# Performance work log

Hardware: AMD Instinct MI355X
Metric: run time of the kernel (lower is better)

## Reference

```python
import jax, jax.numpy as jnp
import numpy as np

D, HID, C = 300, 64, 21          # Dict_size, hidden_size, cell_size
B, H, W = 4, 144, 144

def gelu(x):
    return jax.nn.gelu(x, approximate=False)  # torch nn.GELU default (erf)

def c1x1(x, w, b):
    # 1x1 conv == pointwise matmul over channels: x [b,c,h,w], w [o,c], b [o]
    return jnp.einsum('bchw,oc->bohw', x, w) + b[None, :, None, None]

def gconv(x, w, b):
    return gelu(c1x1(x, w, b))


def setup_inputs() -> dict:
    key = jax.random.key(0)
    ks = iter(jax.random.split(key, 40))
    def Wm(o, i):
        return jax.random.normal(next(ks), (o, i), jnp.float32) * 0.05
    def bv(o):
        return jax.random.normal(next(ks), (o,), jnp.float32) * 0.01
    inp = {'y': jax.random.normal(next(ks), (B, C, H, W), jnp.float32)}
    # cell_size -> Dict_size encoders
    for nm in ['we1', 'we2', 'wfy1', 'wiy1', 'wfy2', 'wiy2']:
        inp[nm + '_w'] = Wm(D, C); inp[nm + '_b'] = bv(D)
    # Dict_size -> Dict_size recurrent convs
    for nm in ['wd1', 'wd2', 'wfx1', 'wix1', 'wfx2', 'wix2']:
        inp[nm + '_w'] = Wm(D, D); inp[nm + '_b'] = bv(D)
    # Line1 head: 3x3 valid conv D->2*HID, then 1x1 2*HID->2*HID, 1x1 2*HID->1
    inp['line_w1'] = jax.random.normal(next(ks), (2 * HID, D, 3, 3), jnp.float32) * 0.05
    inp['line_b1'] = bv(2 * HID)
    inp['line_w2'] = Wm(2 * HID, 2 * HID); inp['line_b2'] = bv(2 * HID)
    inp['line_w3'] = Wm(1, 2 * HID);       inp['line_b3'] = bv(1)
    return inp


def reference(y, we1_w, we1_b, we2_w, we2_b, wfy1_w, wfy1_b, wiy1_w, wiy1_b,
              wfy2_w, wfy2_b, wiy2_w, wiy2_b, wd1_w, wd1_b, wd2_w, wd2_b,
              wfx1_w, wfx1_b, wix1_w, wix1_b, wfx2_w, wfx2_b, wix2_w, wix2_b,
              line_w1, line_b1, line_w2, line_b2, line_w3, line_b3):
    ywe1 = gconv(y, we1_w, we1_b)
    ywe2 = gconv(y, we2_w, we2_b)
    ywfy1 = gconv(y, wfy1_w, wfy1_b)
    ywiy1 = gconv(y, wiy1_w, wiy1_b)
    ywfy2 = gconv(y, wfy2_w, wfy2_b)
    ywiy2 = gconv(y, wiy2_w, wiy2_b)

    def step2(x12, c12, xt1):  # first half-cell (the '2' gates)
        ctlide1 = ywe2 + xt1 - gconv(x12, wd2_w, wd2_b)
        ft1 = jax.nn.sigmoid(gconv(x12, wfx2_w, wfx2_b) + ywfy2)
        it1 = jax.nn.sigmoid(gconv(x12, wix2_w, wix2_b) + ywiy2)
        ct1 = c12 * ft1 + ctlide1 * it1
        return ct1, jax.nn.relu(ct1)

    xt1 = jnp.float32(0.0)
    c12 = jax.nn.sigmoid(ywiy1) * (-ywe1)
    x12 = jax.nn.relu(c12)

    for _ in range(3):
        ct1, xt1 = step2(x12, c12, xt1)
        c1tlide = ywe1 + xt1 - gconv(xt1, wd1_w, wd1_b)
        ft21 = jax.nn.sigmoid(gconv(xt1, wfx1_w, wfx1_b) + ywfy1)
        it21 = jax.nn.sigmoid(gconv(xt1, wix1_w, wix1_b) + ywiy1)
        ct2 = ct1 * ft21 + c1tlide * it21
        x12 = jax.nn.relu(ct2)
        c12 = ct2

    ct1, xt1 = step2(x12, c12, xt1)

    # Line1: 3x3 valid conv + GELU, 1x1 + GELU, 1x1
    h = jax.lax.conv_general_dilated(
        xt1, line_w1, window_strides=(1, 1), padding='VALID',
        dimension_numbers=('NCHW', 'OIHW', 'NCHW')) + line_b1[None, :, None, None]
    h = gelu(h)
    h = gelu(c1x1(h, line_w2, line_b2))
    return c1x1(h, line_w3, line_b3)
```

## Files before the change

kernel.cpp:

```cpp
#include <hip/hip_runtime.h>

typedef _Float16 f16;
typedef _Float16 f16x8 __attribute__((ext_vector_type(8)));
typedef _Float16 f16x4 __attribute__((ext_vector_type(4)));
typedef float    f32x4 __attribute__((ext_vector_type(4)));

#define NP      82944
#define NPIX_B  20736
#define KP      320
#define OC      128
#define NP2     80656
#define NOC     15
#define OCH     20

__device__ __forceinline__ float geluf(float x) {
    return 0.5f * x * (1.0f + erff(x * 0.70710678118654752f));
}
__device__ __forceinline__ float sigm(float x) {
    return 1.0f / (1.0f + __expf(-x));
}
__device__ __forceinline__ f32x4 mfma16(f16x8 a, f16x8 b, f32x4 c) {
    return __builtin_amdgcn_mfma_f32_16x16x32_f16(a, b, c, 0, 0, 0);
}
__device__ __forceinline__ void gload_lds16(const void* g, void* l) {
    __builtin_amdgcn_global_load_lds(
        (const __attribute__((address_space(1))) void*)g,
        (__attribute__((address_space(3))) void*)l, 16, 0, 0);
}
__device__ __forceinline__ int xcd_swz(int bid, int nwg) {
    int q = nwg >> 3, r = nwg & 7;
    int xcd = bid & 7, idx = bid >> 3;
    return (xcd < r ? xcd * (q + 1) : r * (q + 1) + (xcd - r) * q) + idx;
}

__global__ __launch_bounds__(64) void pack_gate_w(
    const float* __restrict__ wd2, const float* __restrict__ wfx2, const float* __restrict__ wix2,
    const float* __restrict__ wd1, const float* __restrict__ wfx1, const float* __restrict__ wix1,
    const float* __restrict__ bd2, const float* __restrict__ bfx2, const float* __restrict__ bix2,
    const float* __restrict__ bd1, const float* __restrict__ bfx1, const float* __restrict__ bix1,
    f16* __restrict__ wpk2, f16* __restrict__ wpk1,
    float* __restrict__ bpk2, float* __restrict__ bpk1)
{
    int bid = blockIdx.x;
    int o = bid % KP;
    int g = (bid / KP) % 3;
    int s = bid / (KP * 3);
    const float* wsrc; const float* bsrc;
    if (s == 0) { wsrc = (g==0)?wd2:((g==1)?wfx2:wix2); bsrc = (g==0)?bd2:((g==1)?bfx2:bix2); }
    else        { wsrc = (g==0)?wd1:((g==1)?wfx1:wix1); bsrc = (g==0)?bd1:((g==1)?bfx1:bix1); }
    f16* wdst = (s==0 ? wpk2 : wpk1) + ((size_t)g*KP + o)*KP;
    int t = threadIdx.x;
#pragma unroll
    for (int i = 0; i < 5; ++i) {
        int k = i*64 + t;
        wdst[k] = (o < 300 && k < 300) ? (f16)wsrc[o*300 + k] : (f16)0.0f;
    }
    if (t == 0) {
        float* bd = (s==0 ? bpk2 : bpk1);
        bd[g*KP + o] = (o < 300) ? bsrc[o] : 0.0f;
    }
}

__global__ __launch_bounds__(64) void pack_line_w(
    const float* __restrict__ lw1, const float* __restrict__ lw2,
    f16* __restrict__ w1p, f16* __restrict__ w2p)
{
    int bid = blockIdx.x;
    int t = threadIdx.x;
    if (bid < 9*OC) {
        int t9 = bid / OC, oc = bid % OC;
        f16* dst = w1p + ((size_t)t9*OC + oc)*KP;
#pragma unroll
        for (int i = 0; i < 5; ++i) {
            int k = i*64 + t;
            dst[k] = (k < 300) ? (f16)lw1[(size_t)(oc*300 + k)*9 + t9] : (f16)0.0f;
        }
    } else {
        int oc = bid - 9*OC;
        f16* dst = w2p + (size_t)oc*OC;
#pragma unroll
        for (int i = 0; i < 2; ++i) {
            int k = i*64 + t;
            dst[k] = (f16)lw2[oc*OC + k];
        }
    }
}

__global__ __launch_bounds__(256) void encoder_kernel(
    const float* __restrict__ y,
    const float* __restrict__ w_e1, const float* __restrict__ b_e1,
    const float* __restrict__ w_e2, const float* __restrict__ b_e2,
    const float* __restrict__ w_f1, const float* __restrict__ b_f1,
    const float* __restrict__ w_i1, const float* __restrict__ b_i1,
    const float* __restrict__ w_f2, const float* __restrict__ b_f2,
    const float* __restrict__ w_i2, const float* __restrict__ b_i2,
    f16* __restrict__ enc, float* __restrict__ cbuf, f16* __restrict__ xa,
    int p_off, int chpx)
{
    int lid = xcd_swz(blockIdx.x, gridDim.x);
    int oc = lid % NOC;
    int pb = lid / NOC;
    int p  = pb * 256 + threadIdx.x;
    if (p >= chpx) return;
    int o0 = oc * OCH;
    int gp = p_off + p;
    int b = gp / NPIX_B, pin = gp % NPIX_B;
    const float* yb = y + (size_t)b*21*NPIX_B + pin;
    float yv[21];
#pragma unroll
    for (int c = 0; c < 21; ++c) yv[c] = yb[(size_t)c * NPIX_B];

    size_t rowbase = (size_t)p*KP + o0;
    size_t estr = (size_t)chpx*KP;

#define ENC_ONE(W, B, EIDX)                                            \
    {                                                                  \
        f16* dst = enc + (size_t)(EIDX)*estr + rowbase;                \
        _Pragma("unroll 1")                                            \
        for (int rq = 0; rq < 5; ++rq) {                               \
            f16x4 st;                                                  \
            _Pragma("unroll")                                          \
            for (int j = 0; j < 4; ++j) {                              \
                int r = rq*4 + j;                                      \
                const float* wr = (W) + (o0 + r)*21;                   \
                float acc = (B)[o0 + r];                               \
                _Pragma("unroll")                                      \
                for (int c = 0; c < 21; ++c) acc = fmaf(wr[c], yv[c], acc); \
                st[j] = (f16)geluf(acc);                               \
            }                                                          \
            *(f16x4*)(dst + rq*4) = st;                                \
        }                                                              \
    }

    ENC_ONE(w_e1, b_e1, 0)
    ENC_ONE(w_e2, b_e2, 1)
    ENC_ONE(w_f1, b_f1, 2)
    ENC_ONE(w_i1, b_i1, 3)
    ENC_ONE(w_f2, b_f2, 4)
    ENC_ONE(w_i2, b_i2, 5)
#undef ENC_ONE

#pragma unroll 1
    for (int rq = 0; rq < 5; ++rq) {
        f16x4 v0 = *(const f16x4*)(enc + (size_t)0*estr + rowbase + rq*4);
        f16x4 v3 = *(const f16x4*)(enc + (size_t)3*estr + rowbase + rq*4);
        f32x4 cv; f16x4 xv;
#pragma unroll
        for (int j = 0; j < 4; ++j) {
            float c12 = sigm((float)v3[j]) * (-(float)v0[j]);
            cv[j] = c12;
            xv[j] = (f16)fmaxf(c12, 0.0f);
        }
        *(f32x4*)(cbuf + rowbase + rq*4) = cv;
        *(f16x4*)(xa + rowbase + rq*4) = xv;
    }
}

__global__ __launch_bounds__(256) void gate_kernel(
    const f16* __restrict__ xin, const f16* __restrict__ wpk,
    const float* __restrict__ bpk,
    const f16* __restrict__ ey, const f16* __restrict__ fy,
    const f16* __restrict__ iy, const f16* __restrict__ ad,
    float* __restrict__ cio, f16* __restrict__ xout, int first, int chpx)
{
    __shared__ char smem[2][28160];
    int tid = threadIdx.x;
    int l = tid & 63, w = tid >> 6;
    int lr = l & 15, lh = l >> 4;
    int lid = xcd_swz(blockIdx.x, gridDim.x);
    int mt = lid % 10, nt = lid / 10;
    int o0 = mt * 32;
    int p0 = nt * 256;

    const char* srcb[7];
#pragma unroll
    for (int j = 0; j < 7; ++j) {
        int c = j*256 + tid;
        if (c < 480) {
            int row = c / 5, slot = c % 5; if (slot > 3) slot = 0;
            int g = row >> 5, o = o0 + (row & 31);
            srcb[j] = (const char*)wpk + ((size_t)g*KP + o)*(KP*2) + slot*16;
        } else if (c < 1760) {
            int cb = c - 480;
            int row = cb / 5, slot = cb % 5; if (slot > 3) slot = 0;
            int p = p0 + row; if (p > chpx-1) p = chpx-1;
            srcb[j] = (const char*)xin + (size_t)p*(KP*2) + slot*16;
        } else srcb[j] = nullptr;
    }

#define GSTAGE(BUF, KS)                                                \
    {                                                                  \
        int kb = (KS)*64;                                              \
        _Pragma("unroll")                                              \
        for (int j = 0; j < 7; ++j) {                                  \
            int c = j*256 + tid;                                       \
            if (c < 1760)                                              \
                gload_lds16(srcb[j] + kb, &smem[BUF][c*16]);           \
        }                                                              \
    }

    f32x4 acc[3][2][4] = {};
    GSTAGE(0, 0)
    __syncthreads();

    int buf = 0;
#pragma unroll 1
    for (int ks = 0; ks < 10; ++ks) {
        if (ks < 9) { GSTAGE(buf^1, ks+1) }
        f16x8 bfr[4];
#pragma unroll
        for (int n = 0; n < 4; ++n)
            bfr[n] = *(const f16x8*)&smem[buf][7680 + (w*64 + n*16 + lr)*80 + lh*16];
#pragma unroll
        for (int g = 0; g < 3; ++g) {
#pragma unroll
            for (int m = 0; m < 2; ++m) {
                f16x8 a = *(const f16x8*)&smem[buf][(g*32 + m*16 + lr)*80 + lh*16];
#pragma unroll
                for (int n = 0; n < 4; ++n)
                    acc[g][m][n] = mfma16(a, bfr[n], acc[g][m][n]);
            }
        }
        __syncthreads();
        buf ^= 1;
    }

#pragma unroll
    for (int m = 0; m < 2; ++m) {
        int o = o0 + m*16 + lh*4;
        if (o >= 300) continue;
        f32x4 bd = *(const f32x4*)(bpk + 0*KP + o);
        f32x4 bf = *(const f32x4*)(bpk + 1*KP + o);
        f32x4 bi = *(const f32x4*)(bpk + 2*KP + o);
#pragma unroll
        for (int n = 0; n < 4; ++n) {
            int p = p0 + w*64 + n*16 + lr;
            if (p >= chpx) continue;
            size_t base = (size_t)p*KP + o;
            f16x4 vey = *(const f16x4*)(ey + base);
            f16x4 vfy = *(const f16x4*)(fy + base);
            f16x4 viy = *(const f16x4*)(iy + base);
            f32x4 vci = *(const f32x4*)(cio + base);
            f16x4 vad = {};
            if (!first) vad = *(const f16x4*)(ad + base);
            f32x4 co; f16x4 xo;
#pragma unroll
            for (int r = 0; r < 4; ++r) {
                float gd = geluf(acc[0][m][n][r] + bd[r]);
                float gf = geluf(acc[1][m][n][r] + bf[r]);
                float gi = geluf(acc[2][m][n][r] + bi[r]);
                float addv = first ? 0.0f : (float)vad[r];
                float ctl = (float)vey[r] + addv - gd;
                float ft  = sigm(gf + (float)vfy[r]);
                float it  = sigm(gi + (float)viy[r]);
                float ct  = vci[r]*ft + ctl*it;
                co[r] = ct;
                xo[r] = (f16)fmaxf(ct, 0.0f);
            }
            *(f32x4*)(cio + base) = co;
            *(f16x4*)(xout + base) = xo;
        }
    }
#undef GSTAGE
}

__global__ __launch_bounds__(256) void conv3_kernel(
    const f16* __restrict__ xt, const f16* __restrict__ w1p,
    const float* __restrict__ b1, f16* __restrict__ h1)
{
    __shared__ char smem[96*656];
    int tid = threadIdx.x;
    int l = tid & 63, w = tid >> 6;
    int lr = l & 15, lh = l >> 4;
    int lid = xcd_swz(blockIdx.x, gridDim.x);
    int xt5 = lid % 5;
    int by  = lid / 5;
    int b = by / 142, yy = by % 142;
    int xw = xt5 * 30;

#pragma unroll
    for (int j = 0; j < 16; ++j) {
        int c = j*256 + tid;
        if (c < 3936) {
            int lrow = c / 41, slot = c % 41; if (slot > 39) slot = 39;
            int dy = lrow >> 5, pxo = lrow & 31;
            int gx = xw + pxo; if (gx > 143) gx = 143;
            size_t gp = (size_t)((b*144 + yy + dy)*144 + gx);
            gload_lds16((const char*)xt + gp*(KP*2) + slot*16, &smem[0] + c*16);
        }
    }
    __syncthreads();

    f32x4 acc[2][2] = {};
#pragma unroll 1
    for (int t9 = 0; t9 < 9; ++t9) {
        int dy = t9 / 3, dx = t9 % 3;
        int r0 = dy*32 + dx + lr;
        int r1 = r0 + 16;
        if (r1 > 95) r1 = 95;
        const f16* ap = w1p + ((size_t)(t9*OC + w*32 + lr))*KP + lh*8;
#pragma unroll
        for (int k0 = 0; k0 < KP; k0 += 32) {
            int kb = (k0>>3)*16 + lh*16;
            f16x8 b0 = *(const f16x8*)&smem[r0*656 + kb];
            f16x8 b1 = *(const f16x8*)&smem[r1*656 + kb];
            f16x8 a0 = *(const f16x8*)(ap + k0);
            f16x8 a1 = *(const f16x8*)(ap + (size_t)16*KP + k0);
            acc[0][0] = mfma16(a0, b0, acc[0][0]);
            acc[0][1] = mfma16(a0, b1, acc[0][1]);
            acc[1][0] = mfma16(a1, b0, acc[1][0]);
            acc[1][1] = mfma16(a1, b1, acc[1][1]);
        }
    }
#pragma unroll
    for (int m = 0; m < 2; ++m) {
        int ocb = w*32 + m*16 + lh*4;
        f32x4 bb = *(const f32x4*)(b1 + ocb);
#pragma unroll
        for (int n = 0; n < 2; ++n) {
            int rel = n*16 + lr;
            int x = xw + rel;
            if (rel < 30 && x < 142) {
                int pout = (b*142 + yy)*142 + x;
                f16x4 hv;
#pragma unroll
                for (int r = 0; r < 4; ++r) hv[r] = (f16)geluf(acc[m][n][r] + bb[r]);
                *(f16x4*)(h1 + (size_t)pout*OC + ocb) = hv;
            }
        }
    }
}

__global__ __launch_bounds__(256) void gemm128_kernel(
    const f16* __restrict__ hin, const f16* __restrict__ w2p,
    const float* __restrict__ b2, f16* __restrict__ hout)
{
    int tid = threadIdx.x;
    int l = tid & 63, w = tid >> 6;
    int lr = l & 15, lh = l >> 4;
    int bid = blockIdx.x;
    int mt = bid & 3, nt = bid >> 2;
    int p0 = nt * 128 + w * 32;
    if (p0 >= NP2) return;
    int o0 = mt * 32;

    f32x4 acc[2][2] = {};
    int pr0 = min(p0 + lr,      NP2 - 1);
    int pr1 = min(p0 + 16 + lr, NP2 - 1);
    const f16* bp0 = hin + (size_t)pr0*OC + lh*8;
    const f16* bp1 = hin + (size_t)pr1*OC + lh*8;
    const f16* ap  = w2p + (size_t)(o0 + lr)*OC + lh*8;
#pragma unroll
    for (int k0 = 0; k0 < OC; k0 += 32) {
        f16x8 b0  = *(const f16x8*)(bp0 + k0);
        f16x8 b1v = *(const f16x8*)(bp1 + k0);
#pragma unroll
        for (int m = 0; m < 2; ++m) {
            f16x8 a = *(const f16x8*)(ap + (size_t)m*16*OC + k0);
            acc[m][0] = mfma16(a, b0,  acc[m][0]);
            acc[m][1] = mfma16(a, b1v, acc[m][1]);
        }
    }
#pragma unroll
    for (int m = 0; m < 2; ++m) {
        int oc = o0 + m*16 + lh*4;
        f32x4 bb = *(const f32x4*)(b2 + oc);
#pragma unroll
        for (int n = 0; n < 2; ++n) {
            int p = p0 + n*16 + lr;
            if (p < NP2) {
                f16x4 hv;
#pragma unroll
                for (int r = 0; r < 4; ++r) hv[r] = (f16)geluf(acc[m][n][r] + bb[r]);
                *(f16x4*)(hout + (size_t)p*OC + oc) = hv;
            }
        }
    }
}

__global__ __launch_bounds__(256) void final_dot_kernel(
    const f16* __restrict__ h2, const float* __restrict__ w3,
    const float* __restrict__ b3, float* __restrict__ out)
{
    int p = blockIdx.x * 256 + threadIdx.x;
    if (p >= NP2) return;
    const f16x8* row = (const f16x8*)(h2 + (size_t)p * OC);
    float acc = 0.0f;
#pragma unroll
    for (int i = 0; i < 16; ++i) {
        f16x8 v = row[i];
#pragma unroll
        for (int j = 0; j < 8; ++j) acc = fmaf((float)v[j], w3[i*8 + j], acc);
    }
    out[p] = acc + b3[0];
}

extern "C" void kernel_launch(void* const* d_in, const int* in_sizes, int n_in,
                              void* d_out, int out_size, void* d_ws, size_t ws_size,
                              hipStream_t stream)
{
    const float* y      = (const float*)d_in[0];
    const float* we1_w  = (const float*)d_in[1];  const float* we1_b  = (const float*)d_in[2];
    const float* we2_w  = (const float*)d_in[3];  const float* we2_b  = (const float*)d_in[4];
    const float* wfy1_w = (const float*)d_in[5];  const float* wfy1_b = (const float*)d_in[6];
    const float* wiy1_w = (const float*)d_in[7];  const float* wiy1_b = (const float*)d_in[8];
    const float* wfy2_w = (const float*)d_in[9];  const float* wfy2_b = (const float*)d_in[10];
    const float* wiy2_w = (const float*)d_in[11]; const float* wiy2_b = (const float*)d_in[12];
    const float* wd1_w  = (const float*)d_in[13]; const float* wd1_b  = (const float*)d_in[14];
    const float* wd2_w  = (const float*)d_in[15]; const float* wd2_b  = (const float*)d_in[16];
    const float* wfx1_w = (const float*)d_in[17]; const float* wfx1_b = (const float*)d_in[18];
    const float* wix1_w = (const float*)d_in[19]; const float* wix1_b = (const float*)d_in[20];
    const float* wfx2_w = (const float*)d_in[21]; const float* wfx2_b = (const float*)d_in[22];
    const float* wix2_w = (const float*)d_in[23]; const float* wix2_b = (const float*)d_in[24];
    const float* line_w1 = (const float*)d_in[25]; const float* line_b1 = (const float*)d_in[26];
    const float* line_w2 = (const float*)d_in[27]; const float* line_b2 = (const float*)d_in[28];
    const float* line_w3 = (const float*)d_in[29]; const float* line_b3 = (const float*)d_in[30];
    float* out = (float*)d_out;

    auto padb = [](size_t b){ return (b + 255) & ~(size_t)255; };
    auto need = [&](int ch)->size_t {
        size_t chpx = (size_t)NP / ch;
        size_t s = 0;
        s += padb(6*chpx*KP*2);
        s += 2*padb(chpx*KP*2);
        s += padb(chpx*KP*4);
        s += padb((size_t)NP*KP*2);
        s += 2*padb((size_t)3*KP*KP*2);
        s += 2*padb((size_t)3*KP*4);
        s += padb((size_t)9*OC*KP*2);
        s += padb((size_t)OC*OC*2);
        return s;
    };
    const int CHN = (need(4) <= ws_size) ? 4 : 8;
    const int chpx = NP / CHN;

    char* base = (char*)d_ws;
    size_t off = 0;
    auto take = [&](size_t bytes) -> void* {
        void* r = base + off;
        off += (bytes + 255) & ~(size_t)255;
        return r;
    };
    char* chunk_base = base;
    f16*   enc  = (f16*)take((size_t)6 * chpx * KP * sizeof(f16));
    f16*   xa   = (f16*)take((size_t)chpx * KP * sizeof(f16));
    f16*   xb   = (f16*)take((size_t)chpx * KP * sizeof(f16));
    float* cbuf = (float*)take((size_t)chpx * KP * sizeof(float));
    f16* xt1full = (f16*)take((size_t)NP * KP * sizeof(f16));
    f16* wpk2 = (f16*)take((size_t)3 * KP * KP * sizeof(f16));
    f16* wpk1 = (f16*)take((size_t)3 * KP * KP * sizeof(f16));
    float* bpk2 = (float*)take((size_t)3 * KP * sizeof(float));
    float* bpk1 = (float*)take((size_t)3 * KP * sizeof(float));
    f16* w1p = (f16*)take((size_t)9 * OC * KP * sizeof(f16));
    f16* w2p = (f16*)take((size_t)OC * OC * sizeof(f16));
    f16* h1 = (f16*)chunk_base;
    f16* h2 = (f16*)(chunk_base + (size_t)NP2 * OC * sizeof(f16));
    if (off > ws_size) return;

    pack_gate_w<<<2*3*KP, 64, 0, stream>>>(wd2_w, wfx2_w, wix2_w, wd1_w, wfx1_w, wix1_w,
                                           wd2_b, wfx2_b, wix2_b, wd1_b, wfx1_b, wix1_b,
                                           wpk2, wpk1, bpk2, bpk1);
    pack_line_w<<<9*OC + OC, 64, 0, stream>>>(line_w1, line_w2, w1p, w2p);

    const int EGRID = ((chpx + 255) / 256) * NOC;
    const int GGRID = ((chpx + 255) / 256) * 10;
    f16* e0 = enc + (size_t)0*chpx*KP;
    f16* e1 = enc + (size_t)1*chpx*KP;
    f16* e2 = enc + (size_t)2*chpx*KP;
    f16* e3 = enc + (size_t)3*chpx*KP;
    f16* e4 = enc + (size_t)4*chpx*KP;
    f16* e5 = enc + (size_t)5*chpx*KP;

    for (int c = 0; c < CHN; ++c) {
        int p_off = c * chpx;
        encoder_kernel<<<EGRID, 256, 0, stream>>>(y,
            we1_w, we1_b, we2_w, we2_b, wfy1_w, wfy1_b, wiy1_w, wiy1_b,
            wfy2_w, wfy2_b, wiy2_w, wiy2_b,
            enc, cbuf, xa, p_off, chpx);

        gate_kernel<<<GGRID, 256, 0, stream>>>(xa, wpk2, bpk2, e1, e4, e5, xb, cbuf, xb, 1, chpx);
        for (int it = 0; it < 3; ++it) {
            gate_kernel<<<GGRID, 256, 0, stream>>>(xb, wpk1, bpk1, e0, e2, e3, xb, cbuf, xa, 0, chpx);
            f16* xo = (it == 2) ? (xt1full + (size_t)p_off * KP) : xb;
            gate_kernel<<<GGRID, 256, 0, stream>>>(xa, wpk2, bpk2, e1, e4, e5, xb, cbuf, xo, 0, chpx);
        }
    }

    conv3_kernel<<<568*5, 256, 0, stream>>>(xt1full, w1p, line_b1, h1);
    gemm128_kernel<<<((NP2 + 127)/128) * 4, 256, 0, stream>>>(h1, w2p, line_b2, h2);
    final_dot_kernel<<<(NP2 + 255)/256, 256, 0, stream>>>(h2, line_w3, line_b3, out);
}
```

Baseline: 2.271 ms.

## Shrink gate tile to 192 pixels with vmcnt pipelining; restructure conv3 K-loop staging

Measured after the change: 2.305 ms. No clear change (+1.5%).

```diff
diff --git a/kernel.cpp b/kernel.cpp
--- a/kernel.cpp
+++ b/kernel.cpp
@@ -12,6 +12,8 @@
 #define NP2     80656
 #define NOC     15
 #define OCH     20
+#define GN      192
+#define GBUF    24576
 
 __device__ __forceinline__ float geluf(float x) {
     return 0.5f * x * (1.0f + erff(x * 0.70710678118654752f));
@@ -163,67 +165,72 @@
     const f16* __restrict__ iy, const f16* __restrict__ ad,
     float* __restrict__ cio, f16* __restrict__ xout, int first, int chpx)
 {
-    __shared__ char smem[2][28160];
+    __shared__ uint4 smem4[2*GBUF/16];
+    char* smem = (char*)smem4;
     int tid = threadIdx.x;
     int l = tid & 63, w = tid >> 6;
     int lr = l & 15, lh = l >> 4;
     int lid = xcd_swz(blockIdx.x, gridDim.x);
     int mt = lid % 10, nt = lid / 10;
     int o0 = mt * 32;
-    int p0 = nt * 256;
-
-    const char* srcb[7];
-#pragma unroll
-    for (int j = 0; j < 7; ++j) {
+    int p0 = nt * GN;
+
+    const char* srcb[6];
+#pragma unroll
+    for (int j = 0; j < 6; ++j) {
         int c = j*256 + tid;
         if (c < 480) {
             int row = c / 5, slot = c % 5; if (slot > 3) slot = 0;
             int g = row >> 5, o = o0 + (row & 31);
             srcb[j] = (const char*)wpk + ((size_t)g*KP + o)*(KP*2) + slot*16;
-        } else if (c < 1760) {
+        } else if (c < 1440) {
             int cb = c - 480;
             int row = cb / 5, slot = cb % 5; if (slot > 3) slot = 0;
-            int p = p0 + row; if (p > chpx-1) p = chpx-1;
-            srcb[j] = (const char*)xin + (size_t)p*(KP*2) + slot*16;
-        } else srcb[j] = nullptr;
+            srcb[j] = (const char*)xin + (size_t)(p0 + row)*(KP*2) + slot*16;
+        } else {
+            srcb[j] = (const char*)xin;
+        }
     }
 
 #define GSTAGE(BUF, KS)                                                \
     {                                                                  \
         int kb = (KS)*64;                                              \
         _Pragma("unroll")                                              \
-        for (int j = 0; j < 7; ++j) {                                  \
-            int c = j*256 + tid;                                       \
-            if (c < 1760)                                              \
-                gload_lds16(srcb[j] + kb, &smem[BUF][c*16]);           \
-        }                                                              \
-    }
-
-    f32x4 acc[3][2][4] = {};
+        for (int j = 0; j < 6; ++j)                                    \
+            gload_lds16(srcb[j] + kb, &smem[(BUF)*GBUF + (j*256+tid)*16]); \
+    }
+
+    f32x4 acc[3][2][3] = {};
     GSTAGE(0, 0)
-    __syncthreads();
 
     int buf = 0;
 #pragma unroll 1
     for (int ks = 0; ks < 10; ++ks) {
-        if (ks < 9) { GSTAGE(buf^1, ks+1) }
-        f16x8 bfr[4];
-#pragma unroll
-        for (int n = 0; n < 4; ++n)
-            bfr[n] = *(const f16x8*)&smem[buf][7680 + (w*64 + n*16 + lr)*80 + lh*16];
+        if (ks < 9) {
+            GSTAGE(buf^1, ks+1)
+            asm volatile("s_waitcnt vmcnt(6)" ::: "memory");
+        } else {
+            asm volatile("s_waitcnt vmcnt(0)" ::: "memory");
+        }
+        __builtin_amdgcn_s_barrier();
+        f16x8 bfr[3];
+#pragma unroll
+        for (int n = 0; n < 3; ++n)
+            bfr[n] = *(const f16x8*)&smem[buf*GBUF + 7680 + (w*48 + n*16 + lr)*80 + lh*16];
 #pragma unroll
         for (int g = 0; g < 3; ++g) {
 #pragma unroll
             for (int m = 0; m < 2; ++m) {
-                f16x8 a = *(const f16x8*)&smem[buf][(g*32 + m*16 + lr)*80 + lh*16];
-#pragma unroll
-                for (int n = 0; n < 4; ++n)
+                f16x8 a = *(const f16x8*)&smem[buf*GBUF + (g*32 + m*16 + lr)*80 + lh*16];
+#pragma unroll
+                for (int n = 0; n < 3; ++n)
                     acc[g][m][n] = mfma16(a, bfr[n], acc[g][m][n]);
             }
         }
-        __syncthreads();
+        if (ks < 9) __builtin_amdgcn_s_barrier();
         buf ^= 1;
     }
+#undef GSTAGE
 
 #pragma unroll
     for (int m = 0; m < 2; ++m) {
@@ -233,8 +240,8 @@
         f32x4 bf = *(const f32x4*)(bpk + 1*KP + o);
         f32x4 bi = *(const f32x4*)(bpk + 2*KP + o);
 #pragma unroll
-        for (int n = 0; n < 4; ++n) {
-            int p = p0 + w*64 + n*16 + lr;
+        for (int n = 0; n < 3; ++n) {
+            int p = p0 + w*48 + n*16 + lr;
             if (p >= chpx) continue;
             size_t base = (size_t)p*KP + o;
             f16x4 vey = *(const f16x4*)(ey + base);
@@ -261,66 +268,81 @@
             *(f16x4*)(xout + base) = xo;
         }
     }
-#undef GSTAGE
 }
 
 __global__ __launch_bounds__(256) void conv3_kernel(
     const f16* __restrict__ xt, const f16* __restrict__ w1p,
     const float* __restrict__ b1, f16* __restrict__ h1)
 {
-    __shared__ char smem[96*656];
+    __shared__ uint4 smem4[750];
+    char* smem = (char*)smem4;
     int tid = threadIdx.x;
     int l = tid & 63, w = tid >> 6;
     int lr = l & 15, lh = l >> 4;
     int lid = xcd_swz(blockIdx.x, gridDim.x);
-    int xt5 = lid % 5;
-    int by  = lid / 5;
+    int xs = lid % 3;
+    int by = lid / 3;
     int b = by / 142, yy = by % 142;
-    int xw = xt5 * 30;
-
-#pragma unroll
-    for (int j = 0; j < 16; ++j) {
+    int x0 = xs * 48;
+
+    const char* sp[3];
+    int dstb[3];
+    bool act[3];
+#pragma unroll
+    for (int j = 0; j < 3; ++j) {
         int c = j*256 + tid;
-        if (c < 3936) {
-            int lrow = c / 41, slot = c % 41; if (slot > 39) slot = 39;
-            int dy = lrow >> 5, pxo = lrow & 31;
-            int gx = xw + pxo; if (gx > 143) gx = 143;
-            size_t gp = (size_t)((b*144 + yy + dy)*144 + gx);
-            gload_lds16((const char*)xt + gp*(KP*2) + slot*16, &smem[0] + c*16);
-        }
-    }
-    __syncthreads();
-
-    f32x4 acc[2][2] = {};
+        act[j] = (c < 600);
+        int cc = act[j] ? c : 599;
+        int row = cc >> 2, slot = cc & 3;
+        int dy = row / 50, pxo = row % 50;
+        int gx = x0 + pxo; if (gx > 143) gx = 143;
+        size_t gp = (size_t)((b*144 + yy + dy)*144 + gx);
+        sp[j] = (const char*)xt + gp*(KP*2) + slot*16;
+        dstb[j] = row*80 + slot*16;
+    }
+
+    uint4 regs[3];
+#pragma unroll
+    for (int j = 0; j < 3; ++j) regs[j] = *(const uint4*)(sp[j]);
+
+    f32x4 acc[2][3] = {};
 #pragma unroll 1
-    for (int t9 = 0; t9 < 9; ++t9) {
-        int dy = t9 / 3, dx = t9 % 3;
-        int r0 = dy*32 + dx + lr;
-        int r1 = r0 + 16;
-        if (r1 > 95) r1 = 95;
-        const f16* ap = w1p + ((size_t)(t9*OC + w*32 + lr))*KP + lh*8;
-#pragma unroll
-        for (int k0 = 0; k0 < KP; k0 += 32) {
-            int kb = (k0>>3)*16 + lh*16;
-            f16x8 b0 = *(const f16x8*)&smem[r0*656 + kb];
-            f16x8 b1 = *(const f16x8*)&smem[r1*656 + kb];
-            f16x8 a0 = *(const f16x8*)(ap + k0);
-            f16x8 a1 = *(const f16x8*)(ap + (size_t)16*KP + k0);
-            acc[0][0] = mfma16(a0, b0, acc[0][0]);
-            acc[0][1] = mfma16(a0, b1, acc[0][1]);
-            acc[1][0] = mfma16(a1, b0, acc[1][0]);
-            acc[1][1] = mfma16(a1, b1, acc[1][1]);
-        }
-    }
+    for (int ks = 0; ks < 10; ++ks) {
+#pragma unroll
+        for (int j = 0; j < 3; ++j)
+            if (act[j]) *(uint4*)&smem[dstb[j]] = regs[j];
+        __syncthreads();
+        if (ks < 9) {
+            int kb = (ks+1)*64;
+#pragma unroll
+            for (int j = 0; j < 3; ++j) regs[j] = *(const uint4*)(sp[j] + kb);
+        }
+        int k0 = ks*32;
+#pragma unroll 3
+        for (int t9 = 0; t9 < 9; ++t9) {
+            int dy = t9 / 3, dx = t9 % 3;
+            const f16* ap = w1p + ((size_t)(t9*OC + w*32 + lr))*KP + k0 + lh*8;
+            f16x8 a0 = *(const f16x8*)ap;
+            f16x8 a1 = *(const f16x8*)(ap + (size_t)16*KP);
+#pragma unroll
+            for (int n = 0; n < 3; ++n) {
+                int row = dy*50 + dx + n*16 + lr;
+                f16x8 bv = *(const f16x8*)&smem[row*80 + lh*16];
+                acc[0][n] = mfma16(a0, bv, acc[0][n]);
+                acc[1][n] = mfma16(a1, bv, acc[1][n]);
+            }
+        }
+        __syncthreads();
+    }
+
 #pragma unroll
     for (int m = 0; m < 2; ++m) {
         int ocb = w*32 + m*16 + lh*4;
         f32x4 bb = *(const f32x4*)(b1 + ocb);
 #pragma unroll
-        for (int n = 0; n < 2; ++n) {
-            int rel = n*16 + lr;
-            int x = xw + rel;
-            if (rel < 30 && x < 142) {
+        for (int n = 0; n < 3; ++n) {
+            int x = x0 + n*16 + lr;
+            if (x < 142) {
                 int pout = (b*142 + yy)*142 + x;
                 f16x4 hv;
 #pragma unroll
@@ -463,7 +485,7 @@
     pack_line_w<<<9*OC + OC, 64, 0, stream>>>(line_w1, line_w2, w1p, w2p);
 
     const int EGRID = ((chpx + 255) / 256) * NOC;
-    const int GGRID = ((chpx + 255) / 256) * 10;
+    const int GGRID = (chpx / GN) * 10;
     f16* e0 = enc + (size_t)0*chpx*KP;
     f16* e1 = enc + (size_t)1*chpx*KP;
     f16* e2 = enc + (size_t)2*chpx*KP;
@@ -486,7 +508,7 @@
         }
     }
 
-    conv3_kernel<<<568*5, 256, 0, stream>>>(xt1full, w1p, line_b1, h1);
+    conv3_kernel<<<568*3, 256, 0, stream>>>(xt1full, w1p, line_b1, h1);
     gemm128_kernel<<<((NP2 + 127)/128) * 4, 256, 0, stream>>>(h1, w2p, line_b2, h2);
     final_dot_kernel<<<(NP2 + 255)/256, 256, 0, stream>>>(h2, line_w3, line_b3, out);
 }
```

## Restructure encoder with shared y staging and retile conv3 over wider pixel strips

Applied to the files above, without the earlier changes.

New measurement: 5.985 ms. +163.5%, slower.

```diff
diff --git a/kernel.cpp b/kernel.cpp
--- a/kernel.cpp
+++ b/kernel.cpp
@@ -10,8 +10,8 @@
 #define KP      320
 #define OC      128
 #define NP2     80656
-#define NOC     15
-#define OCH     20
+#define NOC     10
+#define OCH     32
 
 __device__ __forceinline__ float geluf(float x) {
     return 0.5f * x * (1.0f + erff(x * 0.70710678118654752f));
@@ -97,62 +97,69 @@
     f16* __restrict__ enc, float* __restrict__ cbuf, f16* __restrict__ xa,
     int p_off, int chpx)
 {
+    __shared__ float yv[256][22];
     int lid = xcd_swz(blockIdx.x, gridDim.x);
     int oc = lid % NOC;
     int pb = lid / NOC;
-    int p  = pb * 256 + threadIdx.x;
-    if (p >= chpx) return;
+    int p_base = pb * 256;
     int o0 = oc * OCH;
-    int gp = p_off + p;
-    int b = gp / NPIX_B, pin = gp % NPIX_B;
-    const float* yb = y + (size_t)b*21*NPIX_B + pin;
-    float yv[21];
-#pragma unroll
-    for (int c = 0; c < 21; ++c) yv[c] = yb[(size_t)c * NPIX_B];
-
-    size_t rowbase = (size_t)p*KP + o0;
-    size_t estr = (size_t)chpx*KP;
-
-#define ENC_ONE(W, B, EIDX)                                            \
-    {                                                                  \
-        f16* dst = enc + (size_t)(EIDX)*estr + rowbase;                \
-        _Pragma("unroll 1")                                            \
-        for (int rq = 0; rq < 5; ++rq) {                               \
-            f16x4 st;                                                  \
-            _Pragma("unroll")                                          \
-            for (int j = 0; j < 4; ++j) {                              \
-                int r = rq*4 + j;                                      \
-                const float* wr = (W) + (o0 + r)*21;                   \
-                float acc = (B)[o0 + r];                               \
-                _Pragma("unroll")                                      \
-                for (int c = 0; c < 21; ++c) acc = fmaf(wr[c], yv[c], acc); \
-                st[j] = (f16)geluf(acc);                               \
-            }                                                          \
-            *(f16x4*)(dst + rq*4) = st;                                \
-        }                                                              \
-    }
-
-    ENC_ONE(w_e1, b_e1, 0)
-    ENC_ONE(w_e2, b_e2, 1)
-    ENC_ONE(w_f1, b_f1, 2)
-    ENC_ONE(w_i1, b_i1, 3)
-    ENC_ONE(w_f2, b_f2, 4)
-    ENC_ONE(w_i2, b_i2, 5)
-#undef ENC_ONE
-
+    int t = threadIdx.x;
+    size_t estr = (size_t)chpx * KP;
+
+    {
+        int gp = p_off + p_base + t;
+        if (gp > NP - 1) gp = NP - 1;
+        int b = gp / NPIX_B, pin = gp % NPIX_B;
+        const float* yb = y + (size_t)b*21*NPIX_B + pin;
+#pragma unroll
+        for (int c = 0; c < 21; ++c) yv[t][c] = yb[(size_t)c * NPIX_B];
+    }
+    __syncthreads();
+
+    const float* ws[6] = {w_e1, w_e2, w_f1, w_i1, w_f2, w_i2};
+    const float* bs[6] = {b_e1, b_e2, b_f1, b_i1, b_f2, b_i2};
+
+    int s  = t & 3;
+    int ob = o0 + s*8;
 #pragma unroll 1
-    for (int rq = 0; rq < 5; ++rq) {
-        f16x4 v0 = *(const f16x4*)(enc + (size_t)0*estr + rowbase + rq*4);
-        f16x4 v3 = *(const f16x4*)(enc + (size_t)3*estr + rowbase + rq*4);
-        f32x4 cv; f16x4 xv;
-#pragma unroll
-        for (int j = 0; j < 4; ++j) {
-            float c12 = sigm((float)v3[j]) * (-(float)v0[j]);
-            cv[j] = c12;
+    for (int q = 0; q < 4; ++q) {
+        int pl = q*64 + (t >> 2);
+        int p  = p_base + pl;
+        bool valid = (p < chpx);
+        float yl[21];
+#pragma unroll
+        for (int c = 0; c < 21; ++c) yl[c] = yv[pl][c];
+        size_t rowb = (size_t)p*KP + ob;
+        float g0[8], g3[8];
+#pragma unroll
+        for (int e = 0; e < 6; ++e) {
+            f16x8 st;
+#pragma unroll
+            for (int j = 0; j < 8; ++j) {
+                int r = ob + j; if (r > 299) r = 299;
+                const float* wr = ws[e] + r*21;
+                float acc = bs[e][r];
+#pragma unroll
+                for (int c = 0; c < 21; ++c) acc = fmaf(wr[c], yl[c], acc);
+                float g = geluf(acc);
+                if (e == 0) g0[j] = g;
+                if (e == 3) g3[j] = g;
+                st[j] = (f16)g;
+            }
+            if (valid) *(f16x8*)(enc + (size_t)e*estr + rowb) = st;
+        }
+        f32x4 cv0, cv1; f16x8 xv;
+#pragma unroll
+        for (int j = 0; j < 8; ++j) {
+            float c12 = sigm(g3[j]) * (-g0[j]);
+            if (j < 4) cv0[j] = c12; else cv1[j-4] = c12;
             xv[j] = (f16)fmaxf(c12, 0.0f);
         }
-        *(f32x4*)(cbuf + rowbase + rq*4) = cv;
-        *(f16x4*)(xa + rowbase + rq*4) = xv;
+        if (valid) {
+            *(f32x4*)(cbuf + rowb)     = cv0;
+            *(f32x4*)(cbuf + rowb + 4) = cv1;
+            *(f16x8*)(xa + rowb)       = xv;
+        }
     }
 }
 
@@ -224,6 +231,7 @@
         __syncthreads();
         buf ^= 1;
     }
+#undef GSTAGE
 
 #pragma unroll
     for (int m = 0; m < 2; ++m) {
@@ -261,66 +269,81 @@
             *(f16x4*)(xout + base) = xo;
         }
     }
-#undef GSTAGE
 }
 
 __global__ __launch_bounds__(256) void conv3_kernel(
     const f16* __restrict__ xt, const f16* __restrict__ w1p,
     const float* __restrict__ b1, f16* __restrict__ h1)
 {
-    __shared__ char smem[96*656];
+    __shared__ uint4 smem4[1470];
+    char* smem = (char*)smem4;
     int tid = threadIdx.x;
     int l = tid & 63, w = tid >> 6;
     int lr = l & 15, lh = l >> 4;
     int lid = xcd_swz(blockIdx.x, gridDim.x);
-    int xt5 = lid % 5;
-    int by  = lid / 5;
+    int xs = lid & 1;
+    int by = lid >> 1;
     int b = by / 142, yy = by % 142;
-    int xw = xt5 * 30;
-
-#pragma unroll
-    for (int j = 0; j < 16; ++j) {
+    int x0 = xs * 96;
+
+    const char* sp[5];
+    int dstb[5];
+    bool act[5];
+#pragma unroll
+    for (int j = 0; j < 5; ++j) {
         int c = j*256 + tid;
-        if (c < 3936) {
-            int lrow = c / 41, slot = c % 41; if (slot > 39) slot = 39;
-            int dy = lrow >> 5, pxo = lrow & 31;
-            int gx = xw + pxo; if (gx > 143) gx = 143;
-            size_t gp = (size_t)((b*144 + yy + dy)*144 + gx);
-            gload_lds16((const char*)xt + gp*(KP*2) + slot*16, &smem[0] + c*16);
-        }
-    }
-    __syncthreads();
-
-    f32x4 acc[2][2] = {};
+        act[j] = (c < 1176);
+        int cc = act[j] ? c : 1175;
+        int row = cc >> 2, slot = cc & 3;
+        int dy = row / 98, pxo = row % 98;
+        int gx = x0 + pxo; if (gx > 143) gx = 143;
+        size_t gp = (size_t)((b*144 + yy + dy)*144 + gx);
+        sp[j] = (const char*)xt + gp*(KP*2) + slot*16;
+        dstb[j] = row*80 + slot*16;
+    }
+
+    uint4 regs[5];
+#pragma unroll
+    for (int j = 0; j < 5; ++j) regs[j] = *(const uint4*)(sp[j]);
+
+    f32x4 acc[2][6] = {};
 #pragma unroll 1
-    for (int t9 = 0; t9 < 9; ++t9) {
-        int dy = t9 / 3, dx = t9 % 3;
-        int r0 = dy*32 + dx + lr;
-        int r1 = r0 + 16;
-        if (r1 > 95) r1 = 95;
-        const f16* ap = w1p + ((size_t)(t9*OC + w*32 + lr))*KP + lh*8;
-#pragma unroll
-        for (int k0 = 0; k0 < KP; k0 += 32) {
-            int kb = (k0>>3)*16 + lh*16;
-            f16x8 b0 = *(const f16x8*)&smem[r0*656 + kb];
-            f16x8 b1 = *(const f16x8*)&smem[r1*656 + kb];
-            f16x8 a0 = *(const f16x8*)(ap + k0);
-            f16x8 a1 = *(const f16x8*)(ap + (size_t)16*KP + k0);
-            acc[0][0] = mfma16(a0, b0, acc[0][0]);
-            acc[0][1] = mfma16(a0, b1, acc[0][1]);
-            acc[1][0] = mfma16(a1, b0, acc[1][0]);
-            acc[1][1] = mfma16(a1, b1, acc[1][1]);
-        }
-    }
+    for (int ks = 0; ks < 10; ++ks) {
+#pragma unroll
+        for (int j = 0; j < 5; ++j)
+            if (act[j]) *(uint4*)&smem[dstb[j]] = regs[j];
+        __syncthreads();
+        if (ks < 9) {
+            int kb = (ks+1)*64;
+#pragma unroll
+            for (int j = 0; j < 5; ++j) regs[j] = *(const uint4*)(sp[j] + kb);
+        }
+        int k0 = ks*32;
+#pragma unroll 3
+        for (int t9 = 0; t9 < 9; ++t9) {
+            int dy = t9 / 3, dx = t9 % 3;
+            const f16* ap = w1p + ((size_t)(t9*OC + w*32 + lr))*KP + k0 + lh*8;
+            f16x8 a0 = *(const f16x8*)ap;
+            f16x8 a1 = *(const f16x8*)(ap + (size_t)16*KP);
+#pragma unroll
+            for (int n = 0; n < 6; ++n) {
+                int row = dy*98 + dx + n*16 + lr;
+                f16x8 bv = *(const f16x8*)&smem[row*80 + lh*16];
+                acc[0][n] = mfma16(a0, bv, acc[0][n]);
+                acc[1][n] = mfma16(a1, bv, acc[1][n]);
+            }
+        }
+        __syncthreads();
+    }
+
 #pragma unroll
     for (int m = 0; m < 2; ++m) {
         int ocb = w*32 + m*16 + lh*4;
         f32x4 bb = *(const f32x4*)(b1 + ocb);
 #pragma unroll
-        for (int n = 0; n < 2; ++n) {
-            int rel = n*16 + lr;
-            int x = xw + rel;
-            if (rel < 30 && x < 142) {
+        for (int n = 0; n < 6; ++n) {
+            int x = x0 + n*16 + lr;
+            if (x < 142) {
                 int pout = (b*142 + yy)*142 + x;
                 f16x4 hv;
 #pragma unroll
@@ -486,7 +509,7 @@
         }
     }
 
-    conv3_kernel<<<568*5, 256, 0, stream>>>(xt1full, w1p, line_b1, h1);
+    conv3_kernel<<<568*2, 256, 0, stream>>>(xt1full, w1p, line_b1, h1);
     gemm128_kernel<<<((NP2 + 127)/128) * 4, 256, 0, stream>>>(h1, w2p, line_b2, h2);
     final_dot_kernel<<<(NP2 + 255)/256, 256, 0, stream>>>(h2, line_w3, line_b3, out);
 }
```
